# Optimization experiments

Measured on AMD Instinct MI355X. Metric: run time of the kernel, lower is better.

The kernel has to match this reference:

```python
import jax, jax.numpy as jnp
import numpy as np

DIM = 512
NUM_HEADS = 8
HEAD_DIM = DIM // NUM_HEADS        # 64
L_HEADS = 4                        # int(8 * 0.5)
H_HEADS = NUM_HEADS - L_HEADS      # 4
L_DIM = L_HEADS * HEAD_DIM         # 256
H_DIM = H_HEADS * HEAD_DIM         # 256
WS = 2                             # window_size
SCALE = HEAD_DIM ** -0.5
SEQ_LEN = 1024


def setup_inputs() -> dict:
    key = jax.random.key(0)
    ks = jax.random.split(key, 13)
    B, N, C = 16, 1024, DIM
    def w(k, shape, fan_in):
        return (jax.random.normal(k, shape, jnp.float32) / np.sqrt(fan_in)).astype(jnp.float32)
    return {
        "x": jax.random.normal(ks[0], (B, N, C), jnp.float32),
        "pos_emb": jax.random.normal(ks[1], (1, SEQ_LEN, C), jnp.float32) * 0.02,
        "l_q_w": w(ks[2], (C, L_DIM), C),
        "l_kv_w": w(ks[3], (C, 2 * L_DIM), C),
        "l_proj_w": w(ks[4], (L_DIM, L_DIM), L_DIM),
        "l_proj_b": jax.random.normal(ks[5], (L_DIM,), jnp.float32) * 0.01,
        "h_qkv_w": w(ks[6], (C, 3 * H_DIM), C),
        "h_proj_w": w(ks[7], (H_DIM, H_DIM), H_DIM),
        "h_proj_b": jax.random.normal(ks[8], (H_DIM,), jnp.float32) * 0.01,
        "in_proj_w": w(ks[9], (C, 3 * C), C),
        "in_proj_b": jax.random.normal(ks[10], (3 * C,), jnp.float32) * 0.01,
        "out_proj_w": w(ks[11], (C, C), C),
        "out_proj_b": jax.random.normal(ks[12], (C,), jnp.float32) * 0.01,
        "H": 32,
        "W": 32,
    }


def _hifi(xg, h_qkv_w, h_proj_w, h_proj_b, H, W):
    B, _, _, C = xg.shape
    hg, wg = H // WS, W // WS
    G, T = hg * wg, WS * WS
    # [B, hg, WS, wg, WS, C] -> [B, G, T, C] (window partition)
    xw = xg.reshape(B, hg, WS, wg, WS, C).transpose(0, 1, 3, 2, 4, 5).reshape(B, G, T, C)
    qkv = (xw @ h_qkv_w).reshape(B, G, T, 3, H_HEADS, HEAD_DIM)
    q = qkv[:, :, :, 0].transpose(0, 1, 3, 2, 4)  # [B,G,h,T,d]
    k = qkv[:, :, :, 1].transpose(0, 1, 3, 2, 4)
    v = qkv[:, :, :, 2].transpose(0, 1, 3, 2, 4)
    attn = jax.nn.softmax(jnp.einsum("bghtd,bghsd->bghts", q, k) * SCALE, axis=-1)
    o = jnp.einsum("bghts,bghsd->bghtd", attn, v)
    # window un-partition: [B,G,h,T,d] -> [B,H,W,h_dim]
    o = o.transpose(0, 1, 3, 2, 4).reshape(B, hg, wg, WS, WS, H_DIM)
    o = o.transpose(0, 1, 3, 2, 4, 5).reshape(B, H, W, H_DIM)
    return o @ h_proj_w + h_proj_b


def _lofi(xg, l_q_w, l_kv_w, l_proj_w, l_proj_b, H, W):
    B, _, _, C = xg.shape
    N = H * W
    q = (xg @ l_q_w).reshape(B, N, L_HEADS, HEAD_DIM)
    kv = (xg @ l_kv_w).reshape(B, N, 2, L_HEADS, HEAD_DIM)
    k, v = kv[:, :, 0], kv[:, :, 1]
    attn = jax.nn.softmax(jnp.einsum("bnhd,bmhd->bhnm", q, k) * SCALE, axis=-1)
    o = jnp.einsum("bhnm,bmhd->bnhd", attn, v).reshape(B, H, W, L_DIM)
    return o @ l_proj_w + l_proj_b


def _mha(y, in_proj_w, in_proj_b, out_proj_w, out_proj_b):
    B, N, C = y.shape
    qkv = y @ in_proj_w + in_proj_b
    q, k, v = jnp.split(qkv, 3, axis=-1)
    q = q.reshape(B, N, NUM_HEADS, HEAD_DIM)
    k = k.reshape(B, N, NUM_HEADS, HEAD_DIM)
    v = v.reshape(B, N, NUM_HEADS, HEAD_DIM)
    attn = jax.nn.softmax(jnp.einsum("bnhd,bmhd->bhnm", q, k) * SCALE, axis=-1)
    o = jnp.einsum("bhnm,bmhd->bnhd", attn, v).reshape(B, N, C)
    return o @ out_proj_w + out_proj_b


def reference(x, pos_emb, l_q_w, l_kv_w, l_proj_w, l_proj_b,
              h_qkv_w, h_proj_w, h_proj_b,
              in_proj_w, in_proj_b, out_proj_w, out_proj_b, H, W):
    B, N, C = x.shape
    x = x + pos_emb[:, :N, :]
    xg = x.reshape(B, H, W, C)
    hifi_out = _hifi(xg, h_qkv_w, h_proj_w, h_proj_b, H, W)
    lofi_out = _lofi(xg, l_q_w, l_kv_w, l_proj_w, l_proj_b, H, W)
    y = jnp.concatenate([hifi_out, lofi_out], axis=-1).reshape(B, N, C)
    return _mha(y, in_proj_w, in_proj_b, out_proj_w, out_proj_b)
```

## Files before the change

kernel.cpp:

```cpp
#include <hip/hip_runtime.h>

typedef unsigned short ushort_t;
typedef short bf16x8 __attribute__((ext_vector_type(8)));
typedef float f32x4 __attribute__((ext_vector_type(4)));

#define DEV __device__ __forceinline__

DEV ushort_t f2bf(float f) {
  return (ushort_t)((__float_as_uint(f) + 0x8000u) >> 16);
}
DEV unsigned pk_bf16(float lo, float hi) {
  unsigned a = __float_as_uint(lo) + 0x8000u;
  unsigned b = __float_as_uint(hi) + 0x8000u;
  return __builtin_amdgcn_perm(b, a, 0x07060302);
}
DEV float bf2f(ushort_t h) {
  union { unsigned int u; float f; } v; v.u = ((unsigned int)h) << 16;
  return v.f;
}
DEV f32x4 mfma16(bf16x8 a, bf16x8 b, f32x4 c) {
  return __builtin_amdgcn_mfma_f32_16x16x32_bf16(a, b, c, 0, 0, 0);
}
typedef __attribute__((address_space(3))) void lds_void;
typedef const __attribute__((address_space(1))) void glb_void;
DEV void gl_lds16(const void* g, void* l) {
  __builtin_amdgcn_global_load_lds((glb_void*)g, (lds_void*)l, 16, 0, 0);
}

__global__ __launch_bounds__(256)
void gemm_bt(const ushort_t* __restrict__ A, int lda,
             const ushort_t* __restrict__ BT,
             const float* __restrict__ bias,
             ushort_t* __restrict__ Cb, float* __restrict__ Cf,
             int ldc, int coff, int K, float scv, int sc_lo, int sc_hi)
{
  __shared__ __align__(16) ushort_t As[128 * 32];
  __shared__ __align__(16) ushort_t Bs[128 * 32];
  const int tid  = threadIdx.x;
  const int wave = tid >> 6, lane = tid & 63;
  const int quad = lane >> 4, r16 = lane & 15;
  const int m0 = blockIdx.x * 128, n0 = blockIdx.y * 128;
  const int wm = (wave >> 1) * 64, wn = (wave & 1) * 64;

  f32x4 acc[4][4];
#pragma unroll
  for (int i = 0; i < 4; ++i)
#pragma unroll
    for (int j = 0; j < 4; ++j) acc[i][j] = (f32x4){0.f, 0.f, 0.f, 0.f};

  for (int kc = 0; kc < K; kc += 32) {
#pragma unroll
    for (int p = 0; p < 4; ++p) {
      int wp = p * 4 + wave;
      int lc = ((wp & 7) << 6) + lane;
      int row = lc >> 2, e8 = (lc & 3) * 8;
      if (wp < 8) gl_lds16(&A[(size_t)(m0 + row) * lda + kc + e8], &As[lc * 8]);
      else        gl_lds16(&BT[(size_t)(n0 + row) * K  + kc + e8], &Bs[lc * 8]);
    }
    __syncthreads();
    bf16x8 af[4], bfr[4];
#pragma unroll
    for (int i = 0; i < 4; ++i) {
      af[i]  = *(const bf16x8*)&As[(wm + i * 16 + r16) * 32 + quad * 8];
      bfr[i] = *(const bf16x8*)&Bs[(wn + i * 16 + r16) * 32 + quad * 8];
    }
#pragma unroll
    for (int mi = 0; mi < 4; ++mi)
#pragma unroll
      for (int ni = 0; ni < 4; ++ni)
        acc[mi][ni] = mfma16(af[mi], bfr[ni], acc[mi][ni]);
    __syncthreads();
  }

#pragma unroll
  for (int mi = 0; mi < 4; ++mi) {
#pragma unroll
    for (int ni = 0; ni < 4; ++ni) {
      int col = n0 + wn + ni * 16 + r16;
      float bv = bias ? bias[col] : 0.f;
      float s = (col >= sc_lo && col < sc_hi) ? scv : 1.0f;
#pragma unroll
      for (int r = 0; r < 4; ++r) {
        int row = m0 + wm + mi * 16 + quad * 4 + r;
        float v = (acc[mi][ni][r] + bv) * s;
        if (Cf) Cf[(size_t)row * ldc + coff + col] = v;
        else    Cb[(size_t)row * ldc + coff + col] = f2bf(v);
      }
    }
  }
}

__global__ __launch_bounds__(256)
void flash_attn7(const ushort_t* __restrict__ Q, int qs, int q_ch,
                 const ushort_t* __restrict__ Kg, int ks, int k_ch,
                 const ushort_t* __restrict__ vT,
                 ushort_t* __restrict__ O, int os, int o_ch,
                 int N)
{
  __shared__ __align__(16) ushort_t Ks[2][2][64 * 32];
  __shared__ __align__(16) ushort_t Vs[2][2][64 * 32];

  const int b = blockIdx.z, h = blockIdx.y, H = gridDim.y;
  const int tid = threadIdx.x, wave = tid >> 6, lane = tid & 63;
  const int quad = lane >> 4, c16 = lane & 15;
  const int q0 = blockIdx.x * 128 + wave * 32;

  bf16x8 qf[2][2];
#pragma unroll
  for (int qt = 0; qt < 2; ++qt) {
    const ushort_t* qp = Q + ((size_t)b * N + q0 + qt * 16 + c16) * qs + q_ch + h * 64;
    qf[qt][0] = *(const bf16x8*)&qp[quad * 8];
    qf[qt][1] = *(const bf16x8*)&qp[32 + quad * 8];
  }
  const ushort_t* kbase = Kg + ((size_t)b * N) * ks + k_ch + h * 64;
  const ushort_t* vbase = vT + ((size_t)(b * H + h) * 64) * N;

  f32x4 oacc[2][4];
#pragma unroll
  for (int qt = 0; qt < 2; ++qt)
#pragma unroll
    for (int dt = 0; dt < 4; ++dt) oacc[qt][dt] = (f32x4){0.f, 0.f, 0.f, 0.f};
  float l_acc[2] = {0.f, 0.f};

  const int laneA = (2 * (quad & 1)) * 16 + c16;
  const int laneB = laneA + 16;

  auto stage = [&](int s0, int buf) {
#pragma unroll
    for (int p = 0; p < 4; ++p) {
      int wp = p * 4 + wave;
      int lc = ((wp & 3) << 6) + lane;
      int row = lc >> 2, e8 = (lc & 3) * 8;
      if (wp < 4)       gl_lds16(kbase + (size_t)(s0 + row) * ks + e8,      &Ks[buf][0][lc * 8]);
      else if (wp < 8)  gl_lds16(kbase + (size_t)(s0 + row) * ks + 32 + e8, &Ks[buf][1][lc * 8]);
      else if (wp < 12) gl_lds16(vbase + (size_t)row * N + s0 + e8,         &Vs[buf][0][lc * 8]);
      else              gl_lds16(vbase + (size_t)row * N + s0 + 32 + e8,    &Vs[buf][1][lc * 8]);
    }
  };

  stage(0, 0);
  const int NT = N >> 6;
  for (int it = 0; it < NT; ++it) {
    const int cur = it & 1;
    __syncthreads();
    if (it + 1 < NT) stage((it + 1) << 6, cur ^ 1);

    f32x4 st[4][2];
#pragma unroll
    for (int si = 0; si < 4; ++si) {
      bf16x8 kf0 = *(const bf16x8*)&Ks[cur][0][(si * 16 + c16) * 32 + quad * 8];
      bf16x8 kf1 = *(const bf16x8*)&Ks[cur][1][(si * 16 + c16) * 32 + quad * 8];
#pragma unroll
      for (int qt = 0; qt < 2; ++qt) {
        f32x4 z = (f32x4){0.f, 0.f, 0.f, 0.f};
        z = mfma16(kf0, qf[qt][0], z);
        z = mfma16(kf1, qf[qt][1], z);
        st[si][qt] = z;
      }
    }

#pragma unroll
    for (int qt = 0; qt < 2; ++qt) {
      float tsum = 0.f;
      unsigned pks[4][2];
#pragma unroll
      for (int si = 0; si < 4; ++si) {
        float p0 = __expf(st[si][qt][0]);
        float p1 = __expf(st[si][qt][1]);
        float p2 = __expf(st[si][qt][2]);
        float p3 = __expf(st[si][qt][3]);
        tsum += (p0 + p1) + (p2 + p3);
        pks[si][0] = pk_bf16(p0, p1);
        pks[si][1] = pk_bf16(p2, p3);
      }
      l_acc[qt] += tsum;

      union U8 { bf16x8 f; unsigned u[4]; } pf0, pf1;
      const bool hiq = quad >= 2;
#pragma unroll
      for (int i = 0; i < 4; ++i) {
        int src = (i < 2) ? laneA : laneB;
        unsigned a0 = __shfl(pks[0][i & 1], src);
        unsigned a1 = __shfl(pks[1][i & 1], src);
        unsigned a2 = __shfl(pks[2][i & 1], src);
        unsigned a3 = __shfl(pks[3][i & 1], src);
        pf0.u[i] = hiq ? a1 : a0;
        pf1.u[i] = hiq ? a3 : a2;
      }

#pragma unroll
      for (int dt = 0; dt < 4; ++dt) {
        bf16x8 vf0 = *(const bf16x8*)&Vs[cur][0][(dt * 16 + c16) * 32 + quad * 8];
        bf16x8 vf1 = *(const bf16x8*)&Vs[cur][1][(dt * 16 + c16) * 32 + quad * 8];
        oacc[qt][dt] = mfma16(vf0, pf0.f, oacc[qt][dt]);
        oacc[qt][dt] = mfma16(vf1, pf1.f, oacc[qt][dt]);
      }
    }
  }

#pragma unroll
  for (int qt = 0; qt < 2; ++qt) {
    float l = l_acc[qt];
    l += __shfl_xor(l, 16);
    l += __shfl_xor(l, 32);
    float inv = 1.f / l;
    ushort_t* op = O + ((size_t)b * N + q0 + qt * 16 + c16) * os + o_ch + h * 64;
#pragma unroll
    for (int dt = 0; dt < 4; ++dt) {
      uint2 pkv;
      pkv.x = pk_bf16(oacc[qt][dt][0] * inv, oacc[qt][dt][1] * inv);
      pkv.y = pk_bf16(oacc[qt][dt][2] * inv, oacc[qt][dt][3] * inv);
      *(uint2*)&op[dt * 16 + quad * 4] = pkv;
    }
  }
}

__global__ __launch_bounds__(256)
void transpose_v(const ushort_t* __restrict__ in, int ld, int ch,
                 ushort_t* __restrict__ out, int N, int H)
{
  __shared__ __align__(16) ushort_t T[64][72];
  const int s0 = blockIdx.x * 64, h = blockIdx.y, b = blockIdx.z;
  const int tid = threadIdx.x;
#pragma unroll
  for (int p = 0; p < 2; ++p) {
    int c = p * 256 + tid;
    int sr = c >> 3, d0 = (c & 7) * 8;
    *(uint4*)&T[sr][d0] =
        *(const uint4*)&in[((size_t)b * N + s0 + sr) * ld + ch + h * 64 + d0];
  }
  __syncthreads();
  const int d = tid >> 2, sp = (tid & 3) * 16;
  union { uint4 v; ushort_t u[8]; } A, B;
#pragma unroll
  for (int j = 0; j < 8; ++j) { A.u[j] = T[sp + j][d]; B.u[j] = T[sp + 8 + j][d]; }
  ushort_t* op = out + ((size_t)(b * H + h) * 64 + d) * N + s0 + sp;
  *(uint4*)&op[0] = A.v;
  *(uint4*)&op[8] = B.v;
}

__global__ __launch_bounds__(256)
void hifi_win(const ushort_t* __restrict__ qkv, int ld, ushort_t* __restrict__ out)
{
  const int bg = blockIdx.x;
  const int b = bg >> 8, g = bg & 255;
  const int head = threadIdx.x >> 6, lane = threadIdx.x & 63;
  const int gh = g >> 4, gw = g & 15;

  int n[4];
  float q[4], k[4], v[4];
#pragma unroll
  for (int t = 0; t < 4; ++t) {
    n[t] = (gh * 2 + (t >> 1)) * 32 + gw * 2 + (t & 1);
    size_t base = ((size_t)b * 1024 + n[t]) * ld + head * 64 + lane;
    q[t] = bf2f(qkv[base]);
    k[t] = bf2f(qkv[base + 256]);
    v[t] = bf2f(qkv[base + 512]);
  }
  float sc[4][4];
#pragma unroll
  for (int t = 0; t < 4; ++t)
#pragma unroll
    for (int s = 0; s < 4; ++s) {
      float p = q[t] * k[s];
#pragma unroll
      for (int off = 32; off >= 1; off >>= 1) p += __shfl_xor(p, off);
      sc[t][s] = p * 0.125f;
    }
#pragma unroll
  for (int t = 0; t < 4; ++t) {
    float m = fmaxf(fmaxf(sc[t][0], sc[t][1]), fmaxf(sc[t][2], sc[t][3]));
    float p0 = __expf(sc[t][0] - m), p1 = __expf(sc[t][1] - m);
    float p2 = __expf(sc[t][2] - m), p3 = __expf(sc[t][3] - m);
    float sum = p0 + p1 + p2 + p3;
    float o = (p0 * v[0] + p1 * v[1] + p2 * v[2] + p3 * v[3]) / sum;
    out[((size_t)b * 1024 + n[t]) * 512 + head * 64 + lane] = f2bf(o);
  }
}

struct WEnt { const float* W; ushort_t* WT; int K; int N; };
struct WArgs { WEnt e[7]; };

__global__ __launch_bounds__(256)
void w_prep(WArgs a)
{
  WEnt w = a.e[blockIdx.z];
  if ((int)blockIdx.x >= (w.K >> 6) || (int)blockIdx.y >= (w.N >> 6)) return;
  __shared__ float T[64][65];
  const int k0 = blockIdx.x * 64, n0 = blockIdx.y * 64;
  const int tid = threadIdx.x;
#pragma unroll
  for (int p = 0; p < 4; ++p) {
    int c = p * 256 + tid;
    int kr = c >> 4, f4 = (c & 15) * 4;
    float4 v = *(const float4*)&w.W[(size_t)(k0 + kr) * w.N + n0 + f4];
    T[f4 + 0][kr] = v.x; T[f4 + 1][kr] = v.y;
    T[f4 + 2][kr] = v.z; T[f4 + 3][kr] = v.w;
  }
  __syncthreads();
  const int nl = tid >> 2, kp = (tid & 3) * 16;
  union { uint4 v; ushort_t u[8]; } A, B;
#pragma unroll
  for (int j = 0; j < 8; ++j) {
    A.u[j] = f2bf(T[nl][kp + j]);
    B.u[j] = f2bf(T[nl][kp + 8 + j]);
  }
  ushort_t* op = w.WT + (size_t)(n0 + nl) * w.K + k0 + kp;
  *(uint4*)&op[0] = A.v;
  *(uint4*)&op[8] = B.v;
}

__global__ void add_pos(const float* __restrict__ x, const float* __restrict__ pos,
                        ushort_t* __restrict__ xpe)
{
  int idx = blockIdx.x * 256 + threadIdx.x;
  int e = idx * 4;
  float4 xv = *(const float4*)&x[e];
  float4 pv = *(const float4*)&pos[e & (512 * 1024 - 1)];
  uint2 pk;
  pk.x = pk_bf16(xv.x + pv.x, xv.y + pv.y);
  pk.y = pk_bf16(xv.z + pv.z, xv.w + pv.w);
  *(uint2*)&xpe[e] = pk;
}

extern "C" void kernel_launch(void* const* d_in, const int* in_sizes, int n_in,
                              void* d_out, int out_size, void* d_ws, size_t ws_size,
                              hipStream_t stream)
{
  const float* x         = (const float*)d_in[0];
  const float* pos       = (const float*)d_in[1];
  const float* l_q_w     = (const float*)d_in[2];
  const float* l_kv_w    = (const float*)d_in[3];
  const float* l_proj_w  = (const float*)d_in[4];
  const float* l_proj_b  = (const float*)d_in[5];
  const float* h_qkv_w   = (const float*)d_in[6];
  const float* h_proj_w  = (const float*)d_in[7];
  const float* h_proj_b  = (const float*)d_in[8];
  const float* in_proj_w = (const float*)d_in[9];
  const float* in_proj_b = (const float*)d_in[10];
  const float* out_proj_w= (const float*)d_in[11];
  const float* out_proj_b= (const float*)d_in[12];
  float* out = (float*)d_out;

  const float QSCALE = 0.125f;

  char* ws = (char*)d_ws;
  ushort_t* xpe = (ushort_t*)(ws);
  ushort_t* y   = (ushort_t*)(ws + (size_t)16777216);
  ushort_t* F   = (ushort_t*)(ws + (size_t)33554432);
  ushort_t* rB  = (ushort_t*)(ws + (size_t)83886080);
  ushort_t* wb  = (ushort_t*)(ws + (size_t)100663296);

  ushort_t* F_T      = wb;
  ushort_t* h_projT  = wb + 786432;
  ushort_t* l_projT  = wb + 851968;
  ushort_t* in_projT = wb + 917504;
  ushort_t* out_projT= wb + 1703936;

  const int M = 16384;
  ushort_t* vT_lo = xpe;
  ushort_t* vT_m  = rB;

  WArgs wa;
  wa.e[0] = {h_qkv_w,   F_T,                 512, 768};
  wa.e[1] = {l_q_w,     F_T + 768 * 512,     512, 256};
  wa.e[2] = {l_kv_w,    F_T + 1024 * 512,    512, 512};
  wa.e[3] = {h_proj_w,  h_projT,             256, 256};
  wa.e[4] = {l_proj_w,  l_projT,             256, 256};
  wa.e[5] = {in_proj_w, in_projT,            512, 1536};
  wa.e[6] = {out_proj_w,out_projT,           512, 512};
  w_prep<<<dim3(8, 24, 7), dim3(256), 0, stream>>>(wa);

  add_pos<<<dim3(8192), dim3(256), 0, stream>>>(x, pos, xpe);

  gemm_bt<<<dim3(M / 128, 12), dim3(256), 0, stream>>>(
      xpe, 512, F_T, nullptr, F, nullptr, 1536, 0, 512, QSCALE, 768, 1024);
  hifi_win<<<dim3(4096), dim3(256), 0, stream>>>(F, 1536, rB);
  transpose_v<<<dim3(16, 4, 16), dim3(256), 0, stream>>>(
      F, 1536, 1280, vT_lo, 1024, 4);
  flash_attn7<<<dim3(8, 4, 16), dim3(256), 0, stream>>>(
      F, 1536, 768, F, 1536, 1024, vT_lo, rB, 512, 256, 1024);
  gemm_bt<<<dim3(M / 128, 2), dim3(256), 0, stream>>>(
      rB, 512, h_projT, h_proj_b, y, nullptr, 512, 0, 256, 1.0f, 0, 0);
  gemm_bt<<<dim3(M / 128, 2), dim3(256), 0, stream>>>(
      rB + 256, 512, l_projT, l_proj_b, y, nullptr, 512, 256, 256, 1.0f, 0, 0);
  gemm_bt<<<dim3(M / 128, 12), dim3(256), 0, stream>>>(
      y, 512, in_projT, in_proj_b, F, nullptr, 1536, 0, 512, QSCALE, 0, 512);
  transpose_v<<<dim3(16, 8, 16), dim3(256), 0, stream>>>(
      F, 1536, 1024, vT_m, 1024, 8);
  flash_attn7<<<dim3(8, 8, 16), dim3(256), 0, stream>>>(
      F, 1536, 0, F, 1536, 512, vT_m, xpe, 512, 0, 1024);
  gemm_bt<<<dim3(M / 128, 4), dim3(256), 0, stream>>>(
      xpe, 512, out_projT, out_proj_b, nullptr, out, 512, 0, 512, 1.0f, 0, 0);
}
```

Before: 371.3 us.

## Fold hifi/lofi projections into in_proj weights and split lofi attention across KV

Precomputes combined weights W_c = [h_proj; l_proj] @ in_proj and a combined bias on device, so the two per-branch projection GEMMs over all tokens disappear and the in_proj GEMM reads the raw attention outputs directly. The lofi flash attention, which launched only 512 blocks, is split into two KV slices to double the grid; partial outputs are stored in fp16 with their row sums and merged in a new combine kernel. This adds small weight-prep GEMMs, a combine pass and extra partial-buffer traffic, and changes the rounding path through the fused weights. The partial merge weights by row sums only, which relies on the existing kernel not subtracting a running max.

Measured after the change: 397.9 us. 1.07x slower.

```diff
diff --git a/kernel.cpp b/kernel.cpp
--- a/kernel.cpp
+++ b/kernel.cpp
@@ -17,6 +17,14 @@
 DEV float bf2f(ushort_t h) {
   union { unsigned int u; float f; } v; v.u = ((unsigned int)h) << 16;
   return v.f;
+}
+DEV unsigned pk2_f16(float lo, float hi) {
+  union { _Float16 h; ushort_t u; } a, b;
+  a.h = (_Float16)lo; b.h = (_Float16)hi;
+  return (unsigned)a.u | ((unsigned)b.u << 16);
+}
+DEV float f16f(ushort_t u) {
+  union { ushort_t u; _Float16 h; } v; v.u = u; return (float)v.h;
 }
 DEV f32x4 mfma16(bf16x8 a, bf16x8 b, f32x4 c) {
   return __builtin_amdgcn_mfma_f32_16x16x32_bf16(a, b, c, 0, 0, 0);
@@ -91,11 +99,12 @@
 }
 
 __global__ __launch_bounds__(256)
-void flash_attn7(const ushort_t* __restrict__ Q, int qs, int q_ch,
+void flash_attn8(const ushort_t* __restrict__ Q, int qs, int q_ch,
                  const ushort_t* __restrict__ Kg, int ks, int k_ch,
                  const ushort_t* __restrict__ vT,
                  ushort_t* __restrict__ O, int os, int o_ch,
-                 int N)
+                 ushort_t* __restrict__ Opart, float* __restrict__ lpart,
+                 int N, int nsl)
 {
   __shared__ __align__(16) ushort_t Ks[2][2][64 * 32];
   __shared__ __align__(16) ushort_t Vs[2][2][64 * 32];
@@ -103,7 +112,9 @@
   const int b = blockIdx.z, h = blockIdx.y, H = gridDim.y;
   const int tid = threadIdx.x, wave = tid >> 6, lane = tid & 63;
   const int quad = lane >> 4, c16 = lane & 15;
-  const int q0 = blockIdx.x * 128 + wave * 32;
+  const int qb = blockIdx.x & 7, slice = blockIdx.x >> 3;
+  const int q0 = qb * 128 + wave * 32;
+  const int span = N / nsl, sbeg = slice * span, NT = span >> 6;
 
   bf16x8 qf[2][2];
 #pragma unroll
@@ -138,12 +149,11 @@
     }
   };
 
-  stage(0, 0);
-  const int NT = N >> 6;
+  stage(sbeg, 0);
   for (int it = 0; it < NT; ++it) {
     const int cur = it & 1;
     __syncthreads();
-    if (it + 1 < NT) stage((it + 1) << 6, cur ^ 1);
+    if (it + 1 < NT) stage(sbeg + ((it + 1) << 6), cur ^ 1);
 
     f32x4 st[4][2];
 #pragma unroll
@@ -204,15 +214,50 @@
     l += __shfl_xor(l, 16);
     l += __shfl_xor(l, 32);
     float inv = 1.f / l;
-    ushort_t* op = O + ((size_t)b * N + q0 + qt * 16 + c16) * os + o_ch + h * 64;
-#pragma unroll
-    for (int dt = 0; dt < 4; ++dt) {
-      uint2 pkv;
-      pkv.x = pk_bf16(oacc[qt][dt][0] * inv, oacc[qt][dt][1] * inv);
-      pkv.y = pk_bf16(oacc[qt][dt][2] * inv, oacc[qt][dt][3] * inv);
-      *(uint2*)&op[dt * 16 + quad * 4] = pkv;
-    }
-  }
+    const int q_idx = q0 + qt * 16 + c16;
+    if (Opart) {
+      size_t obase = ((((size_t)slice * 16 + b) * H + h) * 1024 + q_idx) * 64;
+#pragma unroll
+      for (int dt = 0; dt < 4; ++dt) {
+        uint2 w;
+        w.x = pk2_f16(oacc[qt][dt][0] * inv, oacc[qt][dt][1] * inv);
+        w.y = pk2_f16(oacc[qt][dt][2] * inv, oacc[qt][dt][3] * inv);
+        *(uint2*)&Opart[obase + dt * 16 + quad * 4] = w;
+      }
+      if (quad == 0)
+        lpart[(((size_t)slice * 16 + b) * H + h) * 1024 + q_idx] = l;
+    } else {
+      ushort_t* op = O + ((size_t)b * N + q_idx) * os + o_ch + h * 64;
+#pragma unroll
+      for (int dt = 0; dt < 4; ++dt) {
+        uint2 pkv;
+        pkv.x = pk_bf16(oacc[qt][dt][0] * inv, oacc[qt][dt][1] * inv);
+        pkv.y = pk_bf16(oacc[qt][dt][2] * inv, oacc[qt][dt][3] * inv);
+        *(uint2*)&op[dt * 16 + quad * 4] = pkv;
+      }
+    }
+  }
+}
+
+__global__ __launch_bounds__(256)
+void combine_lofi(const ushort_t* __restrict__ Op, const float* __restrict__ lp,
+                  ushort_t* __restrict__ rB)
+{
+  int t = blockIdx.x * 256 + threadIdx.x;
+  int dg = t & 15, q = (t >> 4) & 1023, h = (t >> 14) & 3, b = t >> 16;
+  size_t base = (((size_t)b * 4 + h) * 1024 + q) * 64 + dg * 4;
+  const size_t SL = (size_t)16 * 4 * 1024 * 64;
+  uint2 u0 = *(const uint2*)&Op[base];
+  uint2 u1 = *(const uint2*)&Op[SL + base];
+  size_t li = ((size_t)b * 4 + h) * 1024 + q;
+  float l0 = lp[li], l1 = lp[16 * 4 * 1024 + li];
+  float inv = 1.f / (l0 + l1);
+  float o0 = (f16f(u0.x & 0xffff) * l0 + f16f(u1.x & 0xffff) * l1) * inv;
+  float o1 = (f16f(u0.x >> 16)    * l0 + f16f(u1.x >> 16)    * l1) * inv;
+  float o2 = (f16f(u0.y & 0xffff) * l0 + f16f(u1.y & 0xffff) * l1) * inv;
+  float o3 = (f16f(u0.y >> 16)    * l0 + f16f(u1.y >> 16)    * l1) * inv;
+  uint2 w; w.x = pk_bf16(o0, o1); w.y = pk_bf16(o2, o3);
+  *(uint2*)&rB[((size_t)b * 1024 + q) * 512 + 256 + h * 64 + dg * 4] = w;
 }
 
 __global__ __launch_bounds__(256)
@@ -279,7 +324,7 @@
 }
 
 struct WEnt { const float* W; ushort_t* WT; int K; int N; };
-struct WArgs { WEnt e[7]; };
+struct WArgs { WEnt e[5]; };
 
 __global__ __launch_bounds__(256)
 void w_prep(WArgs a)
@@ -308,6 +353,32 @@
   ushort_t* op = w.WT + (size_t)(n0 + nl) * w.K + k0 + kp;
   *(uint4*)&op[0] = A.v;
   *(uint4*)&op[8] = B.v;
+}
+
+__global__ __launch_bounds__(256)
+void w_cast(const float* __restrict__ A, const float* __restrict__ B,
+            ushort_t* __restrict__ Ab, ushort_t* __restrict__ Bb)
+{
+  int i = blockIdx.x * 256 + threadIdx.x;
+  const float* src = blockIdx.y ? B : A;
+  ushort_t*   dst  = blockIdx.y ? Bb : Ab;
+  int e = i * 4;
+  float4 v = *(const float4*)&src[e];
+  uint2 p; p.x = pk_bf16(v.x, v.y); p.y = pk_bf16(v.z, v.w);
+  *(uint2*)&dst[e] = p;
+}
+
+__global__ __launch_bounds__(256)
+void bprep(const float* __restrict__ bh, const float* __restrict__ bl,
+           const float* __restrict__ bin, const float* __restrict__ Win,
+           float* __restrict__ bc)
+{
+  int n = blockIdx.x * 256 + threadIdx.x;
+  if (n >= 1536) return;
+  float acc = bin[n];
+  for (int c = 0; c < 256; ++c)
+    acc += bh[c] * Win[c * 1536 + n] + bl[c] * Win[(256 + c) * 1536 + n];
+  bc[n] = acc;
 }
 
 __global__ void add_pos(const float* __restrict__ x, const float* __restrict__ pos,
@@ -345,51 +416,56 @@
   const float QSCALE = 0.125f;
 
   char* ws = (char*)d_ws;
-  ushort_t* xpe = (ushort_t*)(ws);
-  ushort_t* y   = (ushort_t*)(ws + (size_t)16777216);
-  ushort_t* F   = (ushort_t*)(ws + (size_t)33554432);
-  ushort_t* rB  = (ushort_t*)(ws + (size_t)83886080);
-  ushort_t* wb  = (ushort_t*)(ws + (size_t)100663296);
+  ushort_t* mhaO = (ushort_t*)(ws);
+  ushort_t* vT_lo= (ushort_t*)(ws);
+  ushort_t* Opart= (ushort_t*)(ws + (size_t)8388608);
+  float*    lpart= (float*)   (ws + (size_t)26214400 - 1048576);
+  ushort_t* Wc_T = (ushort_t*)(ws + (size_t)27262976);
+  float*    bc   = (float*)   (ws + (size_t)29360128);
+  ushort_t* F    = (ushort_t*)(ws + (size_t)33554432);
+  ushort_t* rB   = (ushort_t*)(ws + (size_t)83886080);
+  ushort_t* wb   = (ushort_t*)(ws + (size_t)100663296);
 
   ushort_t* F_T      = wb;
-  ushort_t* h_projT  = wb + 786432;
-  ushort_t* l_projT  = wb + 851968;
-  ushort_t* in_projT = wb + 917504;
-  ushort_t* out_projT= wb + 1703936;
+  ushort_t* in_projT = wb + 786432;
+  ushort_t* out_projT= wb + 1572864;
+  ushort_t* h_projB  = wb + 1835008;
+  ushort_t* l_projB  = wb + 1900544;
+  ushort_t* vT_m     = rB;
 
   const int M = 16384;
-  ushort_t* vT_lo = xpe;
-  ushort_t* vT_m  = rB;
 
   WArgs wa;
-  wa.e[0] = {h_qkv_w,   F_T,                 512, 768};
-  wa.e[1] = {l_q_w,     F_T + 768 * 512,     512, 256};
-  wa.e[2] = {l_kv_w,    F_T + 1024 * 512,    512, 512};
-  wa.e[3] = {h_proj_w,  h_projT,             256, 256};
-  wa.e[4] = {l_proj_w,  l_projT,             256, 256};
-  wa.e[5] = {in_proj_w, in_projT,            512, 1536};
-  wa.e[6] = {out_proj_w,out_projT,           512, 512};
-  w_prep<<<dim3(8, 24, 7), dim3(256), 0, stream>>>(wa);
-
-  add_pos<<<dim3(8192), dim3(256), 0, stream>>>(x, pos, xpe);
+  wa.e[0] = {h_qkv_w,   F_T,              512, 768};
+  wa.e[1] = {l_q_w,     F_T + 768 * 512,  512, 256};
+  wa.e[2] = {l_kv_w,    F_T + 1024 * 512, 512, 512};
+  wa.e[3] = {in_proj_w, in_projT,         512, 1536};
+  wa.e[4] = {out_proj_w,out_projT,        512, 512};
+  w_prep<<<dim3(8, 24, 5), dim3(256), 0, stream>>>(wa);
+  w_cast<<<dim3(64, 2), dim3(256), 0, stream>>>(h_proj_w, l_proj_w, h_projB, l_projB);
+  bprep<<<dim3(6), dim3(256), 0, stream>>>(h_proj_b, l_proj_b, in_proj_b, in_proj_w, bc);
+
+  gemm_bt<<<dim3(12, 2), dim3(256), 0, stream>>>(
+      in_projT, 512, h_projB, nullptr, Wc_T, nullptr, 512, 0, 256, 1.0f, 0, 0);
+  gemm_bt<<<dim3(12, 2), dim3(256), 0, stream>>>(
+      in_projT + 256, 512, l_projB, nullptr, Wc_T, nullptr, 512, 256, 256, 1.0f, 0, 0);
+
+  add_pos<<<dim3(8192), dim3(256), 0, stream>>>(x, pos, (ushort_t*)ws);
 
   gemm_bt<<<dim3(M / 128, 12), dim3(256), 0, stream>>>(
-      xpe, 512, F_T, nullptr, F, nullptr, 1536, 0, 512, QSCALE, 768, 1024);
+      (ushort_t*)ws, 512, F_T, nullptr, F, nullptr, 1536, 0, 512, QSCALE, 768, 1024);
   hifi_win<<<dim3(4096), dim3(256), 0, stream>>>(F, 1536, rB);
   transpose_v<<<dim3(16, 4, 16), dim3(256), 0, stream>>>(
       F, 1536, 1280, vT_lo, 1024, 4);
-  flash_attn7<<<dim3(8, 4, 16), dim3(256), 0, stream>>>(
-      F, 1536, 768, F, 1536, 1024, vT_lo, rB, 512, 256, 1024);
-  gemm_bt<<<dim3(M / 128, 2), dim3(256), 0, stream>>>(
-      rB, 512, h_projT, h_proj_b, y, nullptr, 512, 0, 256, 1.0f, 0, 0);
-  gemm_bt<<<dim3(M / 128, 2), dim3(256), 0, stream>>>(
-      rB + 256, 512, l_projT, l_proj_b, y, nullptr, 512, 256, 256, 1.0f, 0, 0);
+  flash_attn8<<<dim3(16, 4, 16), dim3(256), 0, stream>>>(
+      F, 1536, 768, F, 1536, 1024, vT_lo, nullptr, 0, 0, Opart, lpart, 1024, 2);
+  combine_lofi<<<dim3(4096), dim3(256), 0, stream>>>(Opart, lpart, rB);
   gemm_bt<<<dim3(M / 128, 12), dim3(256), 0, stream>>>(
-      y, 512, in_projT, in_proj_b, F, nullptr, 1536, 0, 512, QSCALE, 0, 512);
+      rB, 512, Wc_T, bc, F, nullptr, 1536, 0, 512, QSCALE, 0, 512);
   transpose_v<<<dim3(16, 8, 16), dim3(256), 0, stream>>>(
       F, 1536, 1024, vT_m, 1024, 8);
-  flash_attn7<<<dim3(8, 8, 16), dim3(256), 0, stream>>>(
-      F, 1536, 0, F, 1536, 512, vT_m, xpe, 512, 0, 1024);
+  flash_attn8<<<dim3(8, 8, 16), dim3(256), 0, stream>>>(
+      F, 1536, 0, F, 1536, 512, vT_m, mhaO, 512, 0, nullptr, nullptr, 1024, 1);
   gemm_bt<<<dim3(M / 128, 4), dim3(256), 0, stream>>>(
-      xpe, 512, out_projT, out_proj_b, nullptr, out, 512, 0, 512, 1.0f, 0, 0);
-}
+      mhaO, 512, out_projT, out_proj_b, nullptr, out, 512, 0, 512, 1.0f, 0, 0);
+}
```
